# Optimization experiments

Hardware: AMD Instinct MI355X
Metric: run time of the kernel (lower is better)

Reference implementation:

```python
import jax, jax.numpy as jnp
import numpy as np

B, S, D, H = 2, 2048, 1024, 16
HD = D // H  # 64

def setup_inputs() -> dict:
    key = jax.random.key(0)
    ks = jax.random.split(key, 6)
    s = 1.0 / np.sqrt(D)
    return {
        "x": jax.random.normal(ks[0], (B, S, D), dtype=jnp.float32),
        "wq": jax.random.normal(ks[1], (D, D), dtype=jnp.float32) * s,
        "wk": jax.random.normal(ks[2], (D, D), dtype=jnp.float32) * s,
        "wv": jax.random.normal(ks[3], (D, D), dtype=jnp.float32) * s,
        "wo": jax.random.normal(ks[4], (D, D), dtype=jnp.float32) * s,
        "bo": jax.random.normal(ks[5], (D,), dtype=jnp.float32) * 0.01,
    }

def reference(x, wq, wk, wv, wo, bo):
    b, s, _ = x.shape
    # QKV projections (qkvBias=False), reshape to [b, h, s, hd]
    q = (x @ wq).reshape(b, s, H, HD).transpose(0, 2, 1, 3)
    k = (x @ wk).reshape(b, s, H, HD).transpose(0, 2, 1, 3)
    v = (x @ wv).reshape(b, s, H, HD).transpose(0, 2, 1, 3)
    # scores, causal mask (upper triangle -> -inf), scale, softmax
    scores = jnp.einsum('bhqd,bhkd->bhqk', q, k)
    causal = jnp.triu(jnp.ones((s, s), dtype=bool), k=1)
    scores = jnp.where(causal, -jnp.inf, scores) / np.sqrt(HD)
    weights = jax.nn.softmax(scores, axis=-1)  # dropout=0 (eval)
    ctx = jnp.einsum('bhqk,bhkd->bhqd', weights, v)
    ctx = ctx.transpose(0, 2, 1, 3).reshape(b, s, D)
    return ctx @ wo + bo
```

## Files before the change

kernel.cpp:

```cpp
#include <hip/hip_runtime.h>
#include <hip/hip_bf16.h>
#include <math.h>

#define BB 2
#define SS 2048
#define DD 1024
#define HH 16
#define HDIM 64

typedef unsigned short u16;
typedef __attribute__((ext_vector_type(8))) short bfrag;
typedef __attribute__((ext_vector_type(4))) short s16x4;
typedef __attribute__((ext_vector_type(4))) float f32x4;

#define NEG_BIG (-1e30f)
#define QSCALE 0.18033688011112042f

__device__ __forceinline__ u16 f2u(float f) {
    unsigned int u = __builtin_bit_cast(unsigned int, f);
    u += 0x7fffu + ((u >> 16) & 1u);
    return (u16)(u >> 16);
}

__device__ __forceinline__ void async16(const u16* g, u16* l) {
    __builtin_amdgcn_global_load_lds((__attribute__((address_space(1))) void*)g,
                                     (__attribute__((address_space(3))) void*)l,
                                     16, 0, 0);
}

__device__ __forceinline__ f32x4 mfma16(bfrag a, bfrag b, f32x4 c) {
    return __builtin_amdgcn_mfma_f32_16x16x32_bf16(a, b, c, 0, 0, 0);
}

__device__ __forceinline__ f32x4 mfma_pv(s16x4 a, s16x4 b, f32x4 c) {
#if __has_builtin(__builtin_amdgcn_mfma_f32_16x16x16_bf16)
    return __builtin_amdgcn_mfma_f32_16x16x16_bf16(a, b, c, 0, 0, 0);
#elif __has_builtin(__builtin_amdgcn_mfma_f32_16x16x16bf16_1k)
    return __builtin_amdgcn_mfma_f32_16x16x16bf16_1k(a, b, c, 0, 0, 0);
#else
    f32x4 d;
    asm("v_mfma_f32_16x16x16_bf16 %0, %1, %2, %3" : "=v"(d) : "v"(a), "v"(b), "v"(c));
    return d;
#endif
}

__global__ __launch_bounds__(256) void prep_k(
    const float* __restrict__ x,  u16* __restrict__ xb,
    const float* __restrict__ wq, const float* __restrict__ wk,
    const float* __restrict__ wv, const float* __restrict__ wo,
    u16* __restrict__ wT)
{
    const int id = blockIdx.x;
    const int t = threadIdx.x;
    if (id < 2048) {
        int i = (id * 256 + t) * 8;
        float4 a = *(const float4*)(x + i);
        float4 b = *(const float4*)(x + i + 4);
        u16 o[8] = { f2u(a.x), f2u(a.y), f2u(a.z), f2u(a.w),
                     f2u(b.x), f2u(b.y), f2u(b.z), f2u(b.w) };
        *(uint4*)(xb + i) = *(uint4*)o;
        return;
    }
    const int wid = id - 2048;
    const int z = wid >> 8;
    const int kt = wid & 15, nt = (wid >> 4) & 15;
    const float* w = (z == 0) ? wq : (z == 1) ? wk : (z == 2) ? wv : wo;
    u16* o = wT + (size_t)z * DD * DD;
    __shared__ __align__(16) u16 T[64][72];
    const int k0 = kt * 64, n0 = nt * 64;
    {
        int kr = t >> 2, nb = (t & 3) * 16;
        const float4* s4 = (const float4*)(w + (size_t)(k0 + kr) * DD + n0 + nb);
        #pragma unroll
        for (int jj = 0; jj < 4; ++jj) {
            float4 v = s4[jj];
            T[kr][nb + jj*4 + 0] = f2u(v.x);
            T[kr][nb + jj*4 + 1] = f2u(v.y);
            T[kr][nb + jj*4 + 2] = f2u(v.z);
            T[kr][nb + jj*4 + 3] = f2u(v.w);
        }
    }
    __syncthreads();
    {
        int nr = t >> 2, kb = (t & 3) * 16;
        u16 tmp[16];
        #pragma unroll
        for (int j = 0; j < 16; ++j) tmp[j] = T[kb + j][nr];
        *(uint4*)(o + (size_t)(n0 + nr) * DD + k0 + kb)     = ((uint4*)tmp)[0];
        *(uint4*)(o + (size_t)(n0 + nr) * DD + k0 + kb + 8) = ((uint4*)tmp)[1];
    }
}

__global__ __launch_bounds__(256) void gemm_qkv_k(
    const u16* __restrict__ xb, const u16* __restrict__ wT,
    u16* __restrict__ Qo, u16* __restrict__ Ko, u16* __restrict__ Vt)
{
    const u16* wTz = wT + (size_t)blockIdx.z * DD * DD;
    const float osc = (blockIdx.z == 0) ? QSCALE : 1.0f;

    __shared__ __align__(16) u16 As[128 * 64];
    __shared__ __align__(16) u16 Bs[64 * 64];

    const int t = threadIdx.x;
    const int m0 = blockIdx.x * 128, n0 = blockIdx.y * 64;
    const int lane15 = t & 15, quad = (t >> 4) & 3, wave = t >> 6;
    const int wm = wave & 1, wn = wave >> 1;

    int arow[4], acol[4];
    #pragma unroll
    for (int i = 0; i < 4; ++i) {
        int c = t + i * 256;
        arow[i] = c >> 3;
        acol[i] = (c & 7) ^ (arow[i] & 7);
    }
    const int br0 = t >> 3,         bs0 = t & 7;
    const int br1 = (t + 256) >> 3, bs1 = (t + 256) & 7;
    const int bc0 = bs0 ^ (br0 & 7);
    const int bc1 = bs1 ^ (br1 & 7);
    const int ldb = (t & 192) * 8;

    int aoff[4][2], boff[2][2];
    #pragma unroll
    for (int mi = 0; mi < 4; ++mi) {
        int r = wm * 64 + mi * 16 + lane15;
        #pragma unroll
        for (int kh = 0; kh < 2; ++kh)
            aoff[mi][kh] = (r * 8 + ((kh * 4 + quad) ^ (r & 7))) * 8;
    }
    #pragma unroll
    for (int ni = 0; ni < 2; ++ni) {
        int r = wn * 32 + ni * 16 + lane15;
        #pragma unroll
        for (int kh = 0; kh < 2; ++kh)
            boff[ni][kh] = (r * 8 + ((kh * 4 + quad) ^ (r & 7))) * 8;
    }

    f32x4 acc[4][2];
    #pragma unroll
    for (int mi = 0; mi < 4; ++mi)
        #pragma unroll
        for (int ni = 0; ni < 2; ++ni)
            acc[mi][ni] = (f32x4){0.f, 0.f, 0.f, 0.f};

    for (int it = 0; it < 16; ++it) {
        const int k0 = it * 64;
        #pragma unroll
        for (int i = 0; i < 4; ++i)
            async16(xb + (size_t)(m0 + arow[i]) * DD + k0 + acol[i] * 8,
                    As + ldb + i * 2048);
        async16(wTz + (size_t)(n0 + br0) * DD + k0 + bc0 * 8, Bs + ldb);
        async16(wTz + (size_t)(n0 + br1) * DD + k0 + bc1 * 8, Bs + ldb + 2048);
        __syncthreads();
        #pragma unroll
        for (int kh = 0; kh < 2; ++kh) {
            bfrag av[4], bv[2];
            #pragma unroll
            for (int mi = 0; mi < 4; ++mi) av[mi] = *(const bfrag*)(As + aoff[mi][kh]);
            #pragma unroll
            for (int ni = 0; ni < 2; ++ni) bv[ni] = *(const bfrag*)(Bs + boff[ni][kh]);
            #pragma unroll
            for (int mi = 0; mi < 4; ++mi)
                #pragma unroll
                for (int ni = 0; ni < 2; ++ni)
                    acc[mi][ni] = mfma16(av[mi], bv[ni], acc[mi][ni]);
        }
        __syncthreads();
    }

    const int h = n0 >> 6;
    const int bq = m0 >> 11;
    const int ms = m0 & (SS - 1);

    if (blockIdx.z != 2) {
        u16* out = (blockIdx.z == 0) ? Qo : Ko;
        u16* dst = out + (((size_t)(bq * HH + h)) * SS) * HDIM;
        #pragma unroll
        for (int mi = 0; mi < 4; ++mi) {
            #pragma unroll
            for (int r = 0; r < 4; ++r) {
                int s = ms + wm * 64 + mi * 16 + quad * 4 + r;
                #pragma unroll
                for (int ni = 0; ni < 2; ++ni) {
                    int hd = wn * 32 + ni * 16 + lane15;
                    dst[(size_t)s * HDIM + hd] = f2u(acc[mi][ni][r] * osc);
                }
            }
        }
    } else {
        u16* T = As;
        __syncthreads();
        #pragma unroll
        for (int mi = 0; mi < 4; ++mi)
            #pragma unroll
            for (int r = 0; r < 4; ++r) {
                int ml = wm * 64 + mi * 16 + quad * 4 + r;
                #pragma unroll
                for (int ni = 0; ni < 2; ++ni) {
                    int nl = wn * 32 + ni * 16 + lane15;
                    T[nl * 128 + (ml ^ ((nl & 7) << 4))] = f2u(acc[mi][ni][r]);
                }
            }
        __syncthreads();
        u16* dst = Vt + ((size_t)(bq * HH + h)) * (HDIM * SS);
        #pragma unroll
        for (int i = 0; i < 4; ++i) {
            int c = t + i * 256;
            int row = c >> 4;
            int mb  = (c & 15) * 8;
            uint4 val = *(const uint4*)&T[row * 128 + (mb ^ ((row & 7) << 4))];
            *(uint4*)(dst + (size_t)row * SS + ms + mb) = val;
        }
    }
}

__global__ __launch_bounds__(256) void gemm_out_k(
    const u16* __restrict__ ctxb, const u16* __restrict__ woT,
    const float* __restrict__ bo, float* __restrict__ out)
{
    __shared__ __align__(16) u16 As[128 * 64];
    __shared__ __align__(16) u16 Bs[64 * 64];

    const int t = threadIdx.x;
    const int m0 = blockIdx.x * 128, n0 = blockIdx.y * 64;
    const int lane15 = t & 15, quad = (t >> 4) & 3, wave = t >> 6;
    const int wm = wave & 1, wn = wave >> 1;

    int arow[4], acol[4];
    #pragma unroll
    for (int i = 0; i < 4; ++i) {
        int c = t + i * 256;
        arow[i] = c >> 3;
        acol[i] = (c & 7) ^ (arow[i] & 7);
    }
    const int br0 = t >> 3,         bs0 = t & 7;
    const int br1 = (t + 256) >> 3, bs1 = (t + 256) & 7;
    const int bc0 = bs0 ^ (br0 & 7);
    const int bc1 = bs1 ^ (br1 & 7);
    const int ldb = (t & 192) * 8;

    int aoff[4][2], boff[2][2];
    #pragma unroll
    for (int mi = 0; mi < 4; ++mi) {
        int r = wm * 64 + mi * 16 + lane15;
        #pragma unroll
        for (int kh = 0; kh < 2; ++kh)
            aoff[mi][kh] = (r * 8 + ((kh * 4 + quad) ^ (r & 7))) * 8;
    }
    #pragma unroll
    for (int ni = 0; ni < 2; ++ni) {
        int r = wn * 32 + ni * 16 + lane15;
        #pragma unroll
        for (int kh = 0; kh < 2; ++kh)
            boff[ni][kh] = (r * 8 + ((kh * 4 + quad) ^ (r & 7))) * 8;
    }

    f32x4 acc[4][2];
    #pragma unroll
    for (int mi = 0; mi < 4; ++mi)
        #pragma unroll
        for (int ni = 0; ni < 2; ++ni)
            acc[mi][ni] = (f32x4){0.f, 0.f, 0.f, 0.f};

    for (int it = 0; it < 16; ++it) {
        const int k0 = it * 64;
        #pragma unroll
        for (int i = 0; i < 4; ++i)
            async16(ctxb + (size_t)(m0 + arow[i]) * DD + k0 + acol[i] * 8,
                    As + ldb + i * 2048);
        async16(woT + (size_t)(n0 + br0) * DD + k0 + bc0 * 8, Bs + ldb);
        async16(woT + (size_t)(n0 + br1) * DD + k0 + bc1 * 8, Bs + ldb + 2048);
        __syncthreads();
        #pragma unroll
        for (int kh = 0; kh < 2; ++kh) {
            bfrag av[4], bv[2];
            #pragma unroll
            for (int mi = 0; mi < 4; ++mi) av[mi] = *(const bfrag*)(As + aoff[mi][kh]);
            #pragma unroll
            for (int ni = 0; ni < 2; ++ni) bv[ni] = *(const bfrag*)(Bs + boff[ni][kh]);
            #pragma unroll
            for (int mi = 0; mi < 4; ++mi)
                #pragma unroll
                for (int ni = 0; ni < 2; ++ni)
                    acc[mi][ni] = mfma16(av[mi], bv[ni], acc[mi][ni]);
        }
        __syncthreads();
    }

    float bias[2];
    #pragma unroll
    for (int ni = 0; ni < 2; ++ni)
        bias[ni] = bo[n0 + wn * 32 + ni * 16 + lane15];

    #pragma unroll
    for (int mi = 0; mi < 4; ++mi) {
        #pragma unroll
        for (int r = 0; r < 4; ++r) {
            int m = m0 + wm * 64 + mi * 16 + quad * 4 + r;
            #pragma unroll
            for (int ni = 0; ni < 2; ++ni) {
                int n = n0 + wn * 32 + ni * 16 + lane15;
                out[(size_t)m * DD + n] = acc[mi][ni][r] + bias[ni];
            }
        }
    }
}

struct AttnState {
    f32x4 acc_o[4];
    f32x4 acc_s;
};

template<bool MASKED>
__device__ __forceinline__ void qkt_pv(
    const u16* __restrict__ Kc, const u16* __restrict__ Vc,
    const bfrag bq[2], const int koff[2], const int voffb[4],
    bool qhi, int kv0, int qg, int quad4,
    AttnState& st, s16x4 ones4)
{
    f32x4 sT[4];
    #pragma unroll
    for (int ni = 0; ni < 4; ++ni) sT[ni] = (f32x4){0.f, 0.f, 0.f, 0.f};

    bfrag vv[2][4];
    #pragma unroll
    for (int nd = 0; nd < 4; ++nd)
        vv[0][nd] = *(const bfrag*)&Vc[voffb[0] + nd * 1024];

    __builtin_amdgcn_s_setprio(1);
    #pragma unroll
    for (int kh = 0; kh < 2; ++kh)
        #pragma unroll
        for (int ni = 0; ni < 4; ++ni)
            sT[ni] = mfma16(*(const bfrag*)&Kc[koff[kh] + ni * 1024], bq[kh], sT[ni]);
    __builtin_amdgcn_s_setprio(0);

    #pragma unroll
    for (int ni = 0; ni < 4; ++ni) {
        if (ni < 3) {
            #pragma unroll
            for (int nd = 0; nd < 4; ++nd)
                vv[(ni + 1) & 1][nd] = *(const bfrag*)&Vc[voffb[ni + 1] + nd * 1024];
        }
        float pv[4];
        #pragma unroll
        for (int r = 0; r < 4; ++r) {
            float v = sT[ni][r];
            if (MASKED) {
                int kvg = kv0 + ni * 16 + quad4 + r;
                if (kvg > qg) v = NEG_BIG;
            }
            pv[r] = exp2f(v);
        }
        unsigned lo = __builtin_amdgcn_perm(
            __builtin_bit_cast(unsigned, pv[1]),
            __builtin_bit_cast(unsigned, pv[0]), 0x07060302u);
        unsigned hi = __builtin_amdgcn_perm(
            __builtin_bit_cast(unsigned, pv[3]),
            __builtin_bit_cast(unsigned, pv[2]), 0x07060302u);
        s16x4 pf = __builtin_bit_cast(s16x4,
            ((unsigned long long)hi << 32) | (unsigned long long)lo);
        __builtin_amdgcn_s_setprio(1);
        st.acc_s = mfma_pv(ones4, pf, st.acc_s);
        #pragma unroll
        for (int nd = 0; nd < 4; ++nd) {
            bfrag v8 = vv[ni & 1][nd];
            s16x4 vlo = __builtin_shufflevector(v8, v8, 0, 1, 2, 3);
            s16x4 vhi = __builtin_shufflevector(v8, v8, 4, 5, 6, 7);
            s16x4 va = qhi ? vhi : vlo;
            st.acc_o[nd] = mfma_pv(va, pf, st.acc_o[nd]);
        }
        __builtin_amdgcn_s_setprio(0);
    }
}

__global__ __launch_bounds__(256, 4) void attn_k(
    const u16* __restrict__ Q, const u16* __restrict__ K,
    const u16* __restrict__ Vt, u16* __restrict__ ctx)
{
    __shared__ __align__(16) u16 Ks[2][64 * 64];
    __shared__ __align__(16) u16 Vs[2][64 * 64];
    const int t = threadIdx.x;
    const int lane15 = t & 15, quad = (t >> 4) & 3, wave = t >> 6;
    const int bh = blockIdx.x;
    const int yy = (int)blockIdx.y;
    const int y0 = yy & 7, rnd = yy >> 3;
    const int qt = (rnd == 0) ? 31 - y0 : (rnd == 1) ? y0
                 : (rnd == 2) ? 23 - y0 : 8 + y0;
    const int q0 = qt * 64;
    const int b = bh >> 4, h = bh & 15;
    const u16* Qb = Q  + (size_t)bh * SS * HDIM;
    const u16* Kb = K  + (size_t)bh * SS * HDIM;
    const u16* Vb = Vt + (size_t)bh * HDIM * SS;

    const int kr0 = t >> 3,         ks0 = t & 7;
    const int kr1 = (t + 256) >> 3, ks1 = (t + 256) & 7;
    const int kc0 = ks0 ^ (kr0 & 7);
    const int kc1 = ks1 ^ (kr1 & 7);
    const int ldst = (t & 192) * 8;

    async16(Qb + (size_t)(q0 + kr0) * HDIM + kc0 * 8, &Ks[1][ldst]);
    async16(Qb + (size_t)(q0 + kr1) * HDIM + kc1 * 8, &Ks[1][ldst + 2048]);
    async16(Kb + (size_t)kr0 * HDIM + kc0 * 8, &Ks[0][ldst]);
    async16(Kb + (size_t)kr1 * HDIM + kc1 * 8, &Ks[0][ldst + 2048]);
    async16(Vb + (size_t)kr0 * SS + kc0 * 8, &Vs[0][ldst]);
    async16(Vb + (size_t)kr1 * SS + kc1 * 8, &Vs[0][ldst + 2048]);

    const int r7 = lane15 & 7;
    int koff[2];
    #pragma unroll
    for (int kh = 0; kh < 2; ++kh)
        koff[kh] = (lane15 * 8 + ((kh * 4 + quad) ^ r7)) * 8;
    int voffb[4];
    #pragma unroll
    for (int ni = 0; ni < 4; ++ni)
        voffb[ni] = (lane15 * 8 + ((ni * 2 + (quad >> 1)) ^ r7)) * 8;
    const bool qhi = (quad & 1) != 0;

    __syncthreads();
    bfrag bq[2];
    bq[0] = *(const bfrag*)&Ks[1][koff[0] + wave * 1024];
    bq[1] = *(const bfrag*)&Ks[1][koff[1] + wave * 1024];
    __syncthreads();

    s16x4 ones4;
    #pragma unroll
    for (int i = 0; i < 4; ++i) ones4[i] = (short)0x3f80;

    AttnState st;
    st.acc_s = (f32x4){0.f, 0.f, 0.f, 0.f};
    #pragma unroll
    for (int nd = 0; nd < 4; ++nd) st.acc_o[nd] = (f32x4){0.f, 0.f, 0.f, 0.f};

    const int qg = q0 + wave * 16 + lane15;
    const int quad4 = quad * 4;

    for (int kt = 0; kt < qt; ++kt) {
        const int nv0 = (kt + 1) * 64;
        const int pb = (kt + 1) & 1;
        async16(Kb + (size_t)(nv0 + kr0) * HDIM + kc0 * 8, &Ks[pb][ldst]);
        async16(Kb + (size_t)(nv0 + kr1) * HDIM + kc1 * 8, &Ks[pb][ldst + 2048]);
        async16(Vb + (size_t)kr0 * SS + nv0 + kc0 * 8, &Vs[pb][ldst]);
        async16(Vb + (size_t)kr1 * SS + nv0 + kc1 * 8, &Vs[pb][ldst + 2048]);
        qkt_pv<false>(Ks[kt & 1], Vs[kt & 1], bq, koff, voffb,
                      qhi, kt * 64, qg, quad4, st, ones4);
        __syncthreads();
    }
    qkt_pv<true>(Ks[qt & 1], Vs[qt & 1], bq, koff, voffb,
                 qhi, qt * 64, qg, quad4, st, ones4);

    const float inv = 1.f / st.acc_s[0];
    const int srow = q0 + wave * 16 + lane15;
    u16* dst = ctx + ((size_t)b * SS + srow) * DD + h * HDIM + quad4;
    #pragma unroll
    for (int nd = 0; nd < 4; ++nd) {
        uint2 stw;
        stw.x = (unsigned)f2u(st.acc_o[nd][0] * inv) |
                ((unsigned)f2u(st.acc_o[nd][1] * inv) << 16);
        stw.y = (unsigned)f2u(st.acc_o[nd][2] * inv) |
                ((unsigned)f2u(st.acc_o[nd][3] * inv) << 16);
        *(uint2*)(dst + nd * 16) = stw;
    }
}

extern "C" void kernel_launch(void* const* d_in, const int* in_sizes, int n_in,
                              void* d_out, int out_size, void* d_ws, size_t ws_size,
                              hipStream_t stream) {
    const float* x  = (const float*)d_in[0];
    const float* wq = (const float*)d_in[1];
    const float* wk = (const float*)d_in[2];
    const float* wv = (const float*)d_in[3];
    const float* wo = (const float*)d_in[4];
    const float* bo = (const float*)d_in[5];
    float* out = (float*)d_out;

    char* ws = (char*)d_ws;
    const size_t MB8 = (size_t)8 * 1024 * 1024;
    u16* xb  = (u16*)(ws);
    u16* wT  = (u16*)(ws + MB8);
    u16* Qb  = (u16*)(ws + 2 * MB8);
    u16* Kb  = (u16*)(ws + 3 * MB8);
    u16* Vt  = (u16*)(ws + 4 * MB8);
    u16* ctxb = xb;

    prep_k    <<<3072, 256, 0, stream>>>(x, xb, wq, wk, wv, wo, wT);
    gemm_qkv_k<<<dim3(32, 16, 3), 256, 0, stream>>>(xb, wT, Qb, Kb, Vt);
    attn_k    <<<dim3(32, 32), 256, 0, stream>>>(Qb, Kb, Vt, ctxb);
    gemm_out_k<<<dim3(32, 16), 256, 0, stream>>>(ctxb, wT + (size_t)3 * DD * DD, bo, out);
}
```

Baseline: 180.6 us.

## Pair mirrored causal query tiles per block to share K/V tile loads

Each attention block now handles two query tiles (p and 31-p), so every K/V tile loaded to shared memory serves both tiles and the causal work per block is balanced. The grid is halved and launch bounds drop from 4 to 2 blocks per CU to make room for the doubled accumulator registers. The V operand is now read directly from LDS as a 4-element fragment per MFMA instead of being double-buffered in registers, which lowers register pressure but removes that software prefetch. Lower occupancy and fewer blocks in flight may weaken latency hiding.

```diff
diff --git a/kernel.cpp b/kernel.cpp
--- a/kernel.cpp
+++ b/kernel.cpp
@@ -305,26 +305,15 @@
     }
 }
 
-struct AttnState {
-    f32x4 acc_o[4];
-    f32x4 acc_s;
-};
-
 template<bool MASKED>
 __device__ __forceinline__ void qkt_pv(
     const u16* __restrict__ Kc, const u16* __restrict__ Vc,
-    const bfrag bq[2], const int koff[2], const int voffb[4],
-    bool qhi, int kv0, int qg, int quad4,
-    AttnState& st, s16x4 ones4)
+    const bfrag bq[2], const int koff[2], const int voff[4],
+    int kv0, int qg, int quad4, f32x4 acc_o[4], f32x4& acc_s, s16x4 ones4)
 {
     f32x4 sT[4];
     #pragma unroll
     for (int ni = 0; ni < 4; ++ni) sT[ni] = (f32x4){0.f, 0.f, 0.f, 0.f};
-
-    bfrag vv[2][4];
-    #pragma unroll
-    for (int nd = 0; nd < 4; ++nd)
-        vv[0][nd] = *(const bfrag*)&Vc[voffb[0] + nd * 1024];
 
     __builtin_amdgcn_s_setprio(1);
     #pragma unroll
@@ -336,11 +325,6 @@
 
     #pragma unroll
     for (int ni = 0; ni < 4; ++ni) {
-        if (ni < 3) {
-            #pragma unroll
-            for (int nd = 0; nd < 4; ++nd)
-                vv[(ni + 1) & 1][nd] = *(const bfrag*)&Vc[voffb[ni + 1] + nd * 1024];
-        }
         float pv[4];
         #pragma unroll
         for (int r = 0; r < 4; ++r) {
@@ -360,20 +344,16 @@
         s16x4 pf = __builtin_bit_cast(s16x4,
             ((unsigned long long)hi << 32) | (unsigned long long)lo);
         __builtin_amdgcn_s_setprio(1);
-        st.acc_s = mfma_pv(ones4, pf, st.acc_s);
-        #pragma unroll
-        for (int nd = 0; nd < 4; ++nd) {
-            bfrag v8 = vv[ni & 1][nd];
-            s16x4 vlo = __builtin_shufflevector(v8, v8, 0, 1, 2, 3);
-            s16x4 vhi = __builtin_shufflevector(v8, v8, 4, 5, 6, 7);
-            s16x4 va = qhi ? vhi : vlo;
-            st.acc_o[nd] = mfma_pv(va, pf, st.acc_o[nd]);
-        }
+        acc_s = mfma_pv(ones4, pf, acc_s);
+        #pragma unroll
+        for (int nd = 0; nd < 4; ++nd)
+            acc_o[nd] = mfma_pv(*(const s16x4*)&Vc[voff[ni] + nd * 1024],
+                                pf, acc_o[nd]);
         __builtin_amdgcn_s_setprio(0);
     }
 }
 
-__global__ __launch_bounds__(256, 4) void attn_k(
+__global__ __launch_bounds__(256, 2) void attn_k(
     const u16* __restrict__ Q, const u16* __restrict__ K,
     const u16* __restrict__ Vt, u16* __restrict__ ctx)
 {
@@ -382,13 +362,11 @@
     const int t = threadIdx.x;
     const int lane15 = t & 15, quad = (t >> 4) & 3, wave = t >> 6;
     const int bh = blockIdx.x;
-    const int yy = (int)blockIdx.y;
-    const int y0 = yy & 7, rnd = yy >> 3;
-    const int qt = (rnd == 0) ? 31 - y0 : (rnd == 1) ? y0
-                 : (rnd == 2) ? 23 - y0 : 8 + y0;
-    const int q0 = qt * 64;
+    const int p = (int)blockIdx.y;
+    const int qa = 31 - p, qb = p;
+    const int q0a = qa * 64, q0b = qb * 64;
     const int b = bh >> 4, h = bh & 15;
-    const u16* Qb = Q  + (size_t)bh * SS * HDIM;
+    const u16* Qp = Q  + (size_t)bh * SS * HDIM;
     const u16* Kb = K  + (size_t)bh * SS * HDIM;
     const u16* Vb = Vt + (size_t)bh * HDIM * SS;
 
@@ -398,8 +376,10 @@
     const int kc1 = ks1 ^ (kr1 & 7);
     const int ldst = (t & 192) * 8;
 
-    async16(Qb + (size_t)(q0 + kr0) * HDIM + kc0 * 8, &Ks[1][ldst]);
-    async16(Qb + (size_t)(q0 + kr1) * HDIM + kc1 * 8, &Ks[1][ldst + 2048]);
+    async16(Qp + (size_t)(q0a + kr0) * HDIM + kc0 * 8, &Ks[1][ldst]);
+    async16(Qp + (size_t)(q0a + kr1) * HDIM + kc1 * 8, &Ks[1][ldst + 2048]);
+    async16(Qp + (size_t)(q0b + kr0) * HDIM + kc0 * 8, &Vs[1][ldst]);
+    async16(Qp + (size_t)(q0b + kr1) * HDIM + kc1 * 8, &Vs[1][ldst + 2048]);
     async16(Kb + (size_t)kr0 * HDIM + kc0 * 8, &Ks[0][ldst]);
     async16(Kb + (size_t)kr1 * HDIM + kc1 * 8, &Ks[0][ldst + 2048]);
     async16(Vb + (size_t)kr0 * SS + kc0 * 8, &Vs[0][ldst]);
@@ -410,55 +390,85 @@
     #pragma unroll
     for (int kh = 0; kh < 2; ++kh)
         koff[kh] = (lane15 * 8 + ((kh * 4 + quad) ^ r7)) * 8;
-    int voffb[4];
+    int voff[4];
     #pragma unroll
     for (int ni = 0; ni < 4; ++ni)
-        voffb[ni] = (lane15 * 8 + ((ni * 2 + (quad >> 1)) ^ r7)) * 8;
-    const bool qhi = (quad & 1) != 0;
+        voff[ni] = (lane15 * 8 + ((ni * 2 + (quad >> 1)) ^ r7)) * 8 + (quad & 1) * 4;
 
     __syncthreads();
-    bfrag bq[2];
-    bq[0] = *(const bfrag*)&Ks[1][koff[0] + wave * 1024];
-    bq[1] = *(const bfrag*)&Ks[1][koff[1] + wave * 1024];
+    bfrag bqa[2], bqb[2];
+    bqa[0] = *(const bfrag*)&Ks[1][koff[0] + wave * 1024];
+    bqa[1] = *(const bfrag*)&Ks[1][koff[1] + wave * 1024];
+    bqb[0] = *(const bfrag*)&Vs[1][koff[0] + wave * 1024];
+    bqb[1] = *(const bfrag*)&Vs[1][koff[1] + wave * 1024];
     __syncthreads();
 
     s16x4 ones4;
     #pragma unroll
     for (int i = 0; i < 4; ++i) ones4[i] = (short)0x3f80;
 
-    AttnState st;
-    st.acc_s = (f32x4){0.f, 0.f, 0.f, 0.f};
-    #pragma unroll
-    for (int nd = 0; nd < 4; ++nd) st.acc_o[nd] = (f32x4){0.f, 0.f, 0.f, 0.f};
-
-    const int qg = q0 + wave * 16 + lane15;
+    f32x4 accA_o[4], accB_o[4];
+    f32x4 accA_s = (f32x4){0.f, 0.f, 0.f, 0.f};
+    f32x4 accB_s = (f32x4){0.f, 0.f, 0.f, 0.f};
+    #pragma unroll
+    for (int nd = 0; nd < 4; ++nd) {
+        accA_o[nd] = (f32x4){0.f, 0.f, 0.f, 0.f};
+        accB_o[nd] = (f32x4){0.f, 0.f, 0.f, 0.f};
+    }
+
+    const int qga = q0a + wave * 16 + lane15;
+    const int qgb = q0b + wave * 16 + lane15;
     const int quad4 = quad * 4;
 
-    for (int kt = 0; kt < qt; ++kt) {
+    for (int kt = 0; kt < qa; ++kt) {
         const int nv0 = (kt + 1) * 64;
         const int pb = (kt + 1) & 1;
         async16(Kb + (size_t)(nv0 + kr0) * HDIM + kc0 * 8, &Ks[pb][ldst]);
         async16(Kb + (size_t)(nv0 + kr1) * HDIM + kc1 * 8, &Ks[pb][ldst + 2048]);
         async16(Vb + (size_t)kr0 * SS + nv0 + kc0 * 8, &Vs[pb][ldst]);
         async16(Vb + (size_t)kr1 * SS + nv0 + kc1 * 8, &Vs[pb][ldst + 2048]);
-        qkt_pv<false>(Ks[kt & 1], Vs[kt & 1], bq, koff, voffb,
-                      qhi, kt * 64, qg, quad4, st, ones4);
-        __syncthreads();
-    }
-    qkt_pv<true>(Ks[qt & 1], Vs[qt & 1], bq, koff, voffb,
-                 qhi, qt * 64, qg, quad4, st, ones4);
-
-    const float inv = 1.f / st.acc_s[0];
-    const int srow = q0 + wave * 16 + lane15;
-    u16* dst = ctx + ((size_t)b * SS + srow) * DD + h * HDIM + quad4;
-    #pragma unroll
-    for (int nd = 0; nd < 4; ++nd) {
-        uint2 stw;
-        stw.x = (unsigned)f2u(st.acc_o[nd][0] * inv) |
-                ((unsigned)f2u(st.acc_o[nd][1] * inv) << 16);
-        stw.y = (unsigned)f2u(st.acc_o[nd][2] * inv) |
-                ((unsigned)f2u(st.acc_o[nd][3] * inv) << 16);
-        *(uint2*)(dst + nd * 16) = stw;
+        const int cb = kt & 1;
+        qkt_pv<false>(Ks[cb], Vs[cb], bqa, koff, voff,
+                      kt * 64, qga, quad4, accA_o, accA_s, ones4);
+        if (kt < qb) {
+            qkt_pv<false>(Ks[cb], Vs[cb], bqb, koff, voff,
+                          kt * 64, qgb, quad4, accB_o, accB_s, ones4);
+        } else if (kt == qb) {
+            qkt_pv<true>(Ks[cb], Vs[cb], bqb, koff, voff,
+                         kt * 64, qgb, quad4, accB_o, accB_s, ones4);
+        }
+        __syncthreads();
+    }
+    qkt_pv<true>(Ks[qa & 1], Vs[qa & 1], bqa, koff, voff,
+                 qa * 64, qga, quad4, accA_o, accA_s, ones4);
+
+    {
+        const float inv = 1.f / accA_s[0];
+        const int srow = q0a + wave * 16 + lane15;
+        u16* dst = ctx + ((size_t)b * SS + srow) * DD + h * HDIM + quad4;
+        #pragma unroll
+        for (int nd = 0; nd < 4; ++nd) {
+            uint2 stw;
+            stw.x = (unsigned)f2u(accA_o[nd][0] * inv) |
+                    ((unsigned)f2u(accA_o[nd][1] * inv) << 16);
+            stw.y = (unsigned)f2u(accA_o[nd][2] * inv) |
+                    ((unsigned)f2u(accA_o[nd][3] * inv) << 16);
+            *(uint2*)(dst + nd * 16) = stw;
+        }
+    }
+    {
+        const float inv = 1.f / accB_s[0];
+        const int srow = q0b + wave * 16 + lane15;
+        u16* dst = ctx + ((size_t)b * SS + srow) * DD + h * HDIM + quad4;
+        #pragma unroll
+        for (int nd = 0; nd < 4; ++nd) {
+            uint2 stw;
+            stw.x = (unsigned)f2u(accB_o[nd][0] * inv) |
+                    ((unsigned)f2u(accB_o[nd][1] * inv) << 16);
+            stw.y = (unsigned)f2u(accB_o[nd][2] * inv) |
+                    ((unsigned)f2u(accB_o[nd][3] * inv) << 16);
+            *(uint2*)(dst + nd * 16) = stw;
+        }
     }
 }
 
@@ -484,6 +494,6 @@
 
     prep_k    <<<3072, 256, 0, stream>>>(x, xb, wq, wk, wv, wo, wT);
     gemm_qkv_k<<<dim3(32, 16, 3), 256, 0, stream>>>(xb, wT, Qb, Kb, Vt);
-    attn_k    <<<dim3(32, 32), 256, 0, stream>>>(Qb, Kb, Vt, ctxb);
+    attn_k    <<<dim3(32, 16), 256, 0, stream>>>(Qb, Kb, Vt, ctxb);
     gemm_out_k<<<dim3(32, 16), 256, 0, stream>>>(ctxb, wT + (size_t)3 * DD * DD, bo, out);
 }
```

Result: no change. 179.8 us (-0.4%).

## Split long causal query tiles across KV halves and add combine kernel

Applied to the files above, without the earlier changes.

Attention work for query tiles 16-31 is split into two KV-range chunks, each written as unnormalized fp32 partial outputs and row sums, then merged by a new combine kernel. This balances per-block work and raises block count from 1024 to 1536. The output GEMM is also retiled to 64x64 blocks with 128-wide K steps, giving twice as many blocks. In exchange there is an extra kernel launch and extra global traffic for the partials.

```diff
diff --git a/kernel.cpp b/kernel.cpp
--- a/kernel.cpp
+++ b/kernel.cpp
@@ -217,31 +217,24 @@
     const u16* __restrict__ ctxb, const u16* __restrict__ woT,
     const float* __restrict__ bo, float* __restrict__ out)
 {
-    __shared__ __align__(16) u16 As[128 * 64];
-    __shared__ __align__(16) u16 Bs[64 * 64];
+    __shared__ __align__(16) u16 As[2][4096];
+    __shared__ __align__(16) u16 Bs[2][4096];
 
     const int t = threadIdx.x;
-    const int m0 = blockIdx.x * 128, n0 = blockIdx.y * 64;
+    const int m0 = blockIdx.x * 64, n0 = blockIdx.y * 64;
     const int lane15 = t & 15, quad = (t >> 4) & 3, wave = t >> 6;
     const int wm = wave & 1, wn = wave >> 1;
 
-    int arow[4], acol[4];
-    #pragma unroll
-    for (int i = 0; i < 4; ++i) {
-        int c = t + i * 256;
-        arow[i] = c >> 3;
-        acol[i] = (c & 7) ^ (arow[i] & 7);
-    }
     const int br0 = t >> 3,         bs0 = t & 7;
     const int br1 = (t + 256) >> 3, bs1 = (t + 256) & 7;
     const int bc0 = bs0 ^ (br0 & 7);
     const int bc1 = bs1 ^ (br1 & 7);
     const int ldb = (t & 192) * 8;
 
-    int aoff[4][2], boff[2][2];
-    #pragma unroll
-    for (int mi = 0; mi < 4; ++mi) {
-        int r = wm * 64 + mi * 16 + lane15;
+    int aoff[2][2], boff[2][2];
+    #pragma unroll
+    for (int mi = 0; mi < 2; ++mi) {
+        int r = wm * 32 + mi * 16 + lane15;
         #pragma unroll
         for (int kh = 0; kh < 2; ++kh)
             aoff[mi][kh] = (r * 8 + ((kh * 4 + quad) ^ (r & 7))) * 8;
@@ -254,34 +247,39 @@
             boff[ni][kh] = (r * 8 + ((kh * 4 + quad) ^ (r & 7))) * 8;
     }
 
-    f32x4 acc[4][2];
-    #pragma unroll
-    for (int mi = 0; mi < 4; ++mi)
+    f32x4 acc[2][2];
+    #pragma unroll
+    for (int mi = 0; mi < 2; ++mi)
         #pragma unroll
         for (int ni = 0; ni < 2; ++ni)
             acc[mi][ni] = (f32x4){0.f, 0.f, 0.f, 0.f};
 
-    for (int it = 0; it < 16; ++it) {
-        const int k0 = it * 64;
-        #pragma unroll
-        for (int i = 0; i < 4; ++i)
-            async16(ctxb + (size_t)(m0 + arow[i]) * DD + k0 + acol[i] * 8,
-                    As + ldb + i * 2048);
-        async16(woT + (size_t)(n0 + br0) * DD + k0 + bc0 * 8, Bs + ldb);
-        async16(woT + (size_t)(n0 + br1) * DD + k0 + bc1 * 8, Bs + ldb + 2048);
-        __syncthreads();
-        #pragma unroll
-        for (int kh = 0; kh < 2; ++kh) {
-            bfrag av[4], bv[2];
-            #pragma unroll
-            for (int mi = 0; mi < 4; ++mi) av[mi] = *(const bfrag*)(As + aoff[mi][kh]);
-            #pragma unroll
-            for (int ni = 0; ni < 2; ++ni) bv[ni] = *(const bfrag*)(Bs + boff[ni][kh]);
-            #pragma unroll
-            for (int mi = 0; mi < 4; ++mi)
+    for (int it = 0; it < 8; ++it) {
+        const int k0 = it * 128;
+        #pragma unroll
+        for (int hh = 0; hh < 2; ++hh) {
+            const int kh64 = k0 + hh * 64;
+            async16(ctxb + (size_t)(m0 + br0) * DD + kh64 + bc0 * 8, &As[hh][ldb]);
+            async16(ctxb + (size_t)(m0 + br1) * DD + kh64 + bc1 * 8, &As[hh][ldb + 2048]);
+            async16(woT  + (size_t)(n0 + br0) * DD + kh64 + bc0 * 8, &Bs[hh][ldb]);
+            async16(woT  + (size_t)(n0 + br1) * DD + kh64 + bc1 * 8, &Bs[hh][ldb + 2048]);
+        }
+        __syncthreads();
+        #pragma unroll
+        for (int hh = 0; hh < 2; ++hh) {
+            #pragma unroll
+            for (int kh = 0; kh < 2; ++kh) {
+                bfrag av[2], bv[2];
                 #pragma unroll
-                for (int ni = 0; ni < 2; ++ni)
-                    acc[mi][ni] = mfma16(av[mi], bv[ni], acc[mi][ni]);
+                for (int mi = 0; mi < 2; ++mi) av[mi] = *(const bfrag*)&As[hh][aoff[mi][kh]];
+                #pragma unroll
+                for (int ni = 0; ni < 2; ++ni) bv[ni] = *(const bfrag*)&Bs[hh][boff[ni][kh]];
+                #pragma unroll
+                for (int mi = 0; mi < 2; ++mi)
+                    #pragma unroll
+                    for (int ni = 0; ni < 2; ++ni)
+                        acc[mi][ni] = mfma16(av[mi], bv[ni], acc[mi][ni]);
+            }
         }
         __syncthreads();
     }
@@ -292,10 +290,10 @@
         bias[ni] = bo[n0 + wn * 32 + ni * 16 + lane15];
 
     #pragma unroll
-    for (int mi = 0; mi < 4; ++mi) {
+    for (int mi = 0; mi < 2; ++mi) {
         #pragma unroll
         for (int r = 0; r < 4; ++r) {
-            int m = m0 + wm * 64 + mi * 16 + quad * 4 + r;
+            int m = m0 + wm * 32 + mi * 16 + quad * 4 + r;
             #pragma unroll
             for (int ni = 0; ni < 2; ++ni) {
                 int n = n0 + wn * 32 + ni * 16 + lane15;
@@ -375,17 +373,24 @@
 
 __global__ __launch_bounds__(256, 4) void attn_k(
     const u16* __restrict__ Q, const u16* __restrict__ K,
-    const u16* __restrict__ Vt, u16* __restrict__ ctx)
+    const u16* __restrict__ Vt, u16* __restrict__ ctx,
+    float* __restrict__ Pb, float* __restrict__ Sb)
 {
     __shared__ __align__(16) u16 Ks[2][64 * 64];
     __shared__ __align__(16) u16 Vs[2][64 * 64];
     const int t = threadIdx.x;
     const int lane15 = t & 15, quad = (t >> 4) & 3, wave = t >> 6;
-    const int bh = blockIdx.x;
-    const int yy = (int)blockIdx.y;
-    const int y0 = yy & 7, rnd = yy >> 3;
-    const int qt = (rnd == 0) ? 31 - y0 : (rnd == 1) ? y0
-                 : (rnd == 2) ? 23 - y0 : 8 + y0;
+
+    const int idx = (int)blockIdx.x;
+    const int bh = idx & 31;
+    const int task = idx >> 5;
+    int qt, k0, k1, slot = 0;
+    if (task < 16)      { qt = 16 + task;        k0 = 0;  k1 = 16;
+                          slot = (bh * 16 + task) * 2; }
+    else if (task < 32) { qt = 31 - (task - 16); k0 = 16; k1 = qt + 1;
+                          slot = (bh * 16 + (qt - 16)) * 2 + 1; }
+    else                { qt = 15 - (task - 32); k0 = 0;  k1 = qt + 1; }
+
     const int q0 = qt * 64;
     const int b = bh >> 4, h = bh & 15;
     const u16* Qb = Q  + (size_t)bh * SS * HDIM;
@@ -400,10 +405,10 @@
 
     async16(Qb + (size_t)(q0 + kr0) * HDIM + kc0 * 8, &Ks[1][ldst]);
     async16(Qb + (size_t)(q0 + kr1) * HDIM + kc1 * 8, &Ks[1][ldst + 2048]);
-    async16(Kb + (size_t)kr0 * HDIM + kc0 * 8, &Ks[0][ldst]);
-    async16(Kb + (size_t)kr1 * HDIM + kc1 * 8, &Ks[0][ldst + 2048]);
-    async16(Vb + (size_t)kr0 * SS + kc0 * 8, &Vs[0][ldst]);
-    async16(Vb + (size_t)kr1 * SS + kc1 * 8, &Vs[0][ldst + 2048]);
+    async16(Kb + (size_t)(k0 * 64 + kr0) * HDIM + kc0 * 8, &Ks[0][ldst]);
+    async16(Kb + (size_t)(k0 * 64 + kr1) * HDIM + kc1 * 8, &Ks[0][ldst + 2048]);
+    async16(Vb + (size_t)kr0 * SS + k0 * 64 + kc0 * 8, &Vs[0][ldst]);
+    async16(Vb + (size_t)kr1 * SS + k0 * 64 + kc1 * 8, &Vs[0][ldst + 2048]);
 
     const int r7 = lane15 & 7;
     int koff[2];
@@ -434,32 +439,83 @@
     const int qg = q0 + wave * 16 + lane15;
     const int quad4 = quad * 4;
 
-    for (int kt = 0; kt < qt; ++kt) {
+    for (int kt = k0; kt < k1 - 1; ++kt) {
         const int nv0 = (kt + 1) * 64;
-        const int pb = (kt + 1) & 1;
-        async16(Kb + (size_t)(nv0 + kr0) * HDIM + kc0 * 8, &Ks[pb][ldst]);
-        async16(Kb + (size_t)(nv0 + kr1) * HDIM + kc1 * 8, &Ks[pb][ldst + 2048]);
-        async16(Vb + (size_t)kr0 * SS + nv0 + kc0 * 8, &Vs[pb][ldst]);
-        async16(Vb + (size_t)kr1 * SS + nv0 + kc1 * 8, &Vs[pb][ldst + 2048]);
+        const int pbuf = (kt + 1) & 1;
+        async16(Kb + (size_t)(nv0 + kr0) * HDIM + kc0 * 8, &Ks[pbuf][ldst]);
+        async16(Kb + (size_t)(nv0 + kr1) * HDIM + kc1 * 8, &Ks[pbuf][ldst + 2048]);
+        async16(Vb + (size_t)kr0 * SS + nv0 + kc0 * 8, &Vs[pbuf][ldst]);
+        async16(Vb + (size_t)kr1 * SS + nv0 + kc1 * 8, &Vs[pbuf][ldst + 2048]);
         qkt_pv<false>(Ks[kt & 1], Vs[kt & 1], bq, koff, voffb,
                       qhi, kt * 64, qg, quad4, st, ones4);
         __syncthreads();
     }
-    qkt_pv<true>(Ks[qt & 1], Vs[qt & 1], bq, koff, voffb,
-                 qhi, qt * 64, qg, quad4, st, ones4);
-
-    const float inv = 1.f / st.acc_s[0];
-    const int srow = q0 + wave * 16 + lane15;
-    u16* dst = ctx + ((size_t)b * SS + srow) * DD + h * HDIM + quad4;
-    #pragma unroll
-    for (int nd = 0; nd < 4; ++nd) {
-        uint2 stw;
-        stw.x = (unsigned)f2u(st.acc_o[nd][0] * inv) |
-                ((unsigned)f2u(st.acc_o[nd][1] * inv) << 16);
-        stw.y = (unsigned)f2u(st.acc_o[nd][2] * inv) |
-                ((unsigned)f2u(st.acc_o[nd][3] * inv) << 16);
-        *(uint2*)(dst + nd * 16) = stw;
-    }
+    {
+        const int kt = k1 - 1;
+        if (kt == qt)
+            qkt_pv<true>(Ks[kt & 1], Vs[kt & 1], bq, koff, voffb,
+                         qhi, kt * 64, qg, quad4, st, ones4);
+        else
+            qkt_pv<false>(Ks[kt & 1], Vs[kt & 1], bq, koff, voffb,
+                          qhi, kt * 64, qg, quad4, st, ones4);
+    }
+
+    if (task < 32) {
+        float* P = Pb + (size_t)slot * 4096;
+        float* S = Sb + (size_t)slot * 64;
+        const int q = wave * 16 + lane15;
+        if (quad == 0) S[q] = st.acc_s[0];
+        #pragma unroll
+        for (int nd = 0; nd < 4; ++nd) {
+            float4 v = {st.acc_o[nd][0], st.acc_o[nd][1],
+                        st.acc_o[nd][2], st.acc_o[nd][3]};
+            *(float4*)(P + q * 64 + nd * 16 + quad4) = v;
+        }
+    } else {
+        const float inv = 1.f / st.acc_s[0];
+        const int srow = q0 + wave * 16 + lane15;
+        u16* dst = ctx + ((size_t)b * SS + srow) * DD + h * HDIM + quad4;
+        #pragma unroll
+        for (int nd = 0; nd < 4; ++nd) {
+            uint2 stw;
+            stw.x = (unsigned)f2u(st.acc_o[nd][0] * inv) |
+                    ((unsigned)f2u(st.acc_o[nd][1] * inv) << 16);
+            stw.y = (unsigned)f2u(st.acc_o[nd][2] * inv) |
+                    ((unsigned)f2u(st.acc_o[nd][3] * inv) << 16);
+            *(uint2*)(dst + nd * 16) = stw;
+        }
+    }
+}
+
+__global__ __launch_bounds__(256) void combine_k(
+    const float* __restrict__ Pb, const float* __restrict__ Sb,
+    u16* __restrict__ ctx)
+{
+    const int idx = (int)blockIdx.x;
+    const int bh = idx >> 4, qtl = idx & 15;
+    const int qt = 16 + qtl;
+    const int b = bh >> 4, h = bh & 15;
+    const int t = threadIdx.x;
+    const int row = t >> 2, cq = (t & 3) * 16;
+
+    const size_t s0 = (size_t)idx * 2;
+    const float* P0 = Pb + s0 * 4096;
+    const float* P1 = P0 + 4096;
+    const float inv = 1.f / (Sb[s0 * 64 + row] + Sb[(s0 + 1) * 64 + row]);
+
+    u16 o[16];
+    #pragma unroll
+    for (int j = 0; j < 4; ++j) {
+        float4 a  = *(const float4*)(P0 + row * 64 + cq + j * 4);
+        float4 b4 = *(const float4*)(P1 + row * 64 + cq + j * 4);
+        o[j*4+0] = f2u((a.x + b4.x) * inv);
+        o[j*4+1] = f2u((a.y + b4.y) * inv);
+        o[j*4+2] = f2u((a.z + b4.z) * inv);
+        o[j*4+3] = f2u((a.w + b4.w) * inv);
+    }
+    u16* dst = ctx + ((size_t)b * SS + qt * 64 + row) * DD + h * HDIM + cq;
+    *(uint4*)(dst)     = ((uint4*)o)[0];
+    *(uint4*)(dst + 8) = ((uint4*)o)[1];
 }
 
 extern "C" void kernel_launch(void* const* d_in, const int* in_sizes, int n_in,
@@ -474,16 +530,19 @@
     float* out = (float*)d_out;
 
     char* ws = (char*)d_ws;
-    const size_t MB8 = (size_t)8 * 1024 * 1024;
+    const size_t MB = (size_t)1024 * 1024;
     u16* xb  = (u16*)(ws);
-    u16* wT  = (u16*)(ws + MB8);
-    u16* Qb  = (u16*)(ws + 2 * MB8);
-    u16* Kb  = (u16*)(ws + 3 * MB8);
-    u16* Vt  = (u16*)(ws + 4 * MB8);
+    u16* wT  = (u16*)(ws + 8 * MB);
+    u16* Qb  = (u16*)(ws + 16 * MB);
+    u16* Kb  = (u16*)(ws + 24 * MB);
+    u16* Vt  = (u16*)(ws + 32 * MB);
+    float* Pb = (float*)(ws + 40 * MB);
+    float* Sb = (float*)(ws + 56 * MB);
     u16* ctxb = xb;
 
     prep_k    <<<3072, 256, 0, stream>>>(x, xb, wq, wk, wv, wo, wT);
     gemm_qkv_k<<<dim3(32, 16, 3), 256, 0, stream>>>(xb, wT, Qb, Kb, Vt);
-    attn_k    <<<dim3(32, 32), 256, 0, stream>>>(Qb, Kb, Vt, ctxb);
-    gemm_out_k<<<dim3(32, 16), 256, 0, stream>>>(ctxb, wT + (size_t)3 * DD * DD, bo, out);
-}
+    attn_k    <<<1536, 256, 0, stream>>>(Qb, Kb, Vt, ctxb, Pb, Sb);
+    combine_k <<<512, 256, 0, stream>>>(Pb, Sb, ctxb);
+    gemm_out_k<<<dim3(64, 16), 256, 0, stream>>>(ctxb, wT + (size_t)3 * DD * DD, bo, out);
+}
```

Result: no change. 181.8 us (+0.6%).
